# Optimization experiments

Hardware: AMD Instinct MI355X
Metric: run time of the kernel (lower is better)

Reference implementation:

```python
import jax, jax.numpy as jnp
import numpy as np

N_NODES = 50000
N_EDGES = 1_600_000
N_REL = 8
D_IN = 128
D_OUT = 128


def _unique_edges(rng, n_nodes, n_rel, n_edges):
    # Torch module clamps the dense adjacency to 0/1, so duplicate
    # (rel, src, dst) triples collapse; generate unique edges so the
    # edge-list formulation matches exactly.
    m = 2 * n_edges
    src = rng.integers(0, n_nodes, m)
    dst = rng.integers(0, n_nodes, m)
    et = rng.integers(0, n_rel, m)
    key = (et.astype(np.int64) * n_nodes + src) * n_nodes + dst
    _, idx = np.unique(key, return_index=True)
    idx = np.sort(idx)[:n_edges]
    return src[idx], dst[idx], et[idx]


def setup_inputs() -> dict:
    key = jax.random.key(0)
    kx, kw, kr, kb = jax.random.split(key, 4)
    rng = np.random.default_rng(0)
    src, dst, et = _unique_edges(rng, N_NODES, N_REL, N_EDGES)
    bound = 1.0 / np.sqrt(D_OUT)
    return {
        "x": jax.random.normal(kx, (N_NODES, D_IN), dtype=jnp.float32),
        "edge_index": jnp.asarray(np.stack([src, dst]), dtype=jnp.int64),
        "edge_type": jnp.asarray(et, dtype=jnp.int64),
        "weight": jax.random.uniform(kw, (N_REL, D_OUT, D_IN), minval=-bound, maxval=bound, dtype=jnp.float32),
        "root": jax.random.uniform(kr, (D_OUT, D_IN), minval=-bound, maxval=bound, dtype=jnp.float32),
        "bias": jax.random.uniform(kb, (D_OUT,), minval=-bound, maxval=bound, dtype=jnp.float32),
    }


def reference(x, edge_index, edge_type, weight, root, bias):
    # Math identical to: adj[l, src, dst] = 1; adj row-normalized (mean);
    # out = sum_r norm_adj_r @ x @ W_r^T + x @ root^T + bias.
    n_rel, d_out, d_in = weight.shape
    n_nodes = x.shape[0]
    src = edge_index[0]
    dst = edge_index[1]
    seg = (edge_type * n_nodes + src).astype(jnp.int32)  # segment per (rel, node)
    num_seg = n_rel * n_nodes
    # sum of neighbor features per (relation, node): [R*N, d_in]
    agg = jax.ops.segment_sum(x[dst], seg, num_segments=num_seg)
    deg = jax.ops.segment_sum(jnp.ones((src.shape[0],), dtype=x.dtype), seg, num_segments=num_seg)
    norm = jnp.where(deg > 0, 1.0 / deg, 0.0)[:, None]  # mean aggr, nan_to_num(0)
    agg = (agg * norm).reshape(n_rel, n_nodes, d_in)
    out = jnp.einsum('rnd,rod->no', agg, weight)
    out = out + x @ root.T + bias[None]
    return out
```

## Files before the change

kernel.cpp:

```cpp
#include <hip/hip_runtime.h>


#define D 128
#define SCAN_CHUNK 2048
#define SEG_BITS 9
#define SEGS_PER_BUCKET 512
#define NBLK 128
#define NDEG 32

typedef __attribute__((ext_vector_type(8))) short short8;
typedef __attribute__((ext_vector_type(4))) float v4f;
typedef __attribute__((ext_vector_type(2))) float f32x2;
typedef __attribute__((ext_vector_type(4))) unsigned uint4v;

#define GLOAD_LDS16(gptr, lptr) \
    __builtin_amdgcn_global_load_lds((const __attribute__((address_space(1))) void*)(gptr), \
                                     (__attribute__((address_space(3))) void*)(lptr), 16, 0, 0)

__device__ __forceinline__ unsigned short f2b(float f) {
    union { float f; unsigned u; } v; v.f = f;
    unsigned r = v.u + 0x7fffu + ((v.u >> 16) & 1u);
    return (unsigned short)(r >> 16);
}
__device__ __forceinline__ float blo(unsigned u) {
    union { unsigned u; float f; } v; v.u = u << 16; return v.f;
}
__device__ __forceinline__ float bhi(unsigned u) {
    union { unsigned u; float f; } v; v.u = u & 0xffff0000u; return v.f;
}

__global__ void cvt_bf16_all(const float* __restrict__ x, long long nx,
                             const float* __restrict__ w, long long nw,
                             const float* __restrict__ root, long long nr,
                             unsigned short* __restrict__ Abuf,
                             unsigned short* __restrict__ wB, size_t SLs) {
    long long i = ((long long)blockIdx.x * blockDim.x + threadIdx.x) * 4;
    if (i < nx) {
        float4 v = *(const float4*)(x + i);
        uint2 p;
        p.x = (unsigned)f2b(v.x) | ((unsigned)f2b(v.y) << 16);
        p.y = (unsigned)f2b(v.z) | ((unsigned)f2b(v.w) << 16);
        long long n = i >> 7;
        int d = (int)(i & 127);
        size_t o = (size_t)((d >> 5) * 9 + 8) * SLs + (size_t)n * 32 + (d & 31);
        *(uint2*)(Abuf + o) = p;
        return;
    }
    const float* src;
    unsigned short* dst;
    long long j;
    if (i < nx + nw) { src = w; dst = wB; j = i - nx; }
    else if (i < nx + nw + nr) { src = root; dst = wB + nw; j = i - nx - nw; }
    else return;
    float4 v = *(const float4*)(src + j);
    uint2 p;
    p.x = (unsigned)f2b(v.x) | ((unsigned)f2b(v.y) << 16);
    p.y = (unsigned)f2b(v.z) | ((unsigned)f2b(v.w) << 16);
    *(uint2*)(dst + j) = p;
}

__global__ __launch_bounds__(256)
void histA(const int* __restrict__ ei, const int* __restrict__ et,
           int* __restrict__ blockHist, int nE, int nN, int B, int epb) {
    __shared__ int lh[1024];
    const int tid = threadIdx.x;
    for (int b = tid; b < B; b += 256) lh[b] = 0;
    __syncthreads();
    const int base = blockIdx.x * epb;
    const int lim = min(base + epb, nE);
    for (int e = base + tid; e < lim; e += 256) {
        int seg = et[e] * nN + ei[e];
        atomicAdd(&lh[seg >> SEG_BITS], 1);
    }
    __syncthreads();
    for (int b = tid; b < B; b += 256)
        blockHist[b * NBLK + blockIdx.x] = lh[b];
}

__global__ __launch_bounds__(256)
void scan1(const int* __restrict__ in, int* __restrict__ excl,
           int* __restrict__ blockSums, int n) {
    __shared__ int t[256];
    const int tid = threadIdx.x;
    const int base = blockIdx.x * SCAN_CHUNK + tid * 8;
    int v[8];
    int tot = 0;
#pragma unroll
    for (int i = 0; i < 8; i++) {
        v[i] = (base + i < n) ? in[base + i] : 0;
        tot += v[i];
    }
    t[tid] = tot;
    __syncthreads();
    for (int off = 1; off < 256; off <<= 1) {
        int add = (tid >= off) ? t[tid - off] : 0;
        __syncthreads();
        t[tid] += add;
        __syncthreads();
    }
    int run = t[tid] - tot;
#pragma unroll
    for (int i = 0; i < 8; i++) {
        if (base + i < n) excl[base + i] = run;
        run += v[i];
    }
    if (tid == 255) blockSums[blockIdx.x] = t[255];
}

__global__ __launch_bounds__(256)
void scan2(int* __restrict__ blockSums, int nb) {
    __shared__ int t[256];
    const int tid = threadIdx.x;
    int v = (tid < nb) ? blockSums[tid] : 0;
    t[tid] = v;
    __syncthreads();
    for (int off = 1; off < 256; off <<= 1) {
        int add = (tid >= off) ? t[tid - off] : 0;
        __syncthreads();
        t[tid] += add;
        __syncthreads();
    }
    if (tid < nb) blockSums[tid] = t[tid] - v;
}

__global__ __launch_bounds__(256)
void scatterA(const int* __restrict__ ei, const int* __restrict__ et,
              const int* __restrict__ scanned, const int* __restrict__ blockSums,
              unsigned* __restrict__ bucketEdges,
              int nE, int nN, int B, int epb) {
    __shared__ int cur[1024];
    const int tid = threadIdx.x;
    for (int b = tid; b < B; b += 256) {
        int idx = b * NBLK + blockIdx.x;
        cur[b] = scanned[idx] + blockSums[idx >> 11];
    }
    __syncthreads();
    const int base = blockIdx.x * epb;
    const int lim = min(base + epb, nE);
    for (int e = base + tid; e < lim; e += 256) {
        int seg = et[e] * nN + ei[e];
        int bkt = seg >> SEG_BITS;
        unsigned pk = ((unsigned)(seg & (SEGS_PER_BUCKET - 1)) << 16) | (unsigned)ei[nE + e];
        int pos = atomicAdd(&cur[bkt], 1);
        bucketEdges[pos] = pk;
    }
}

__global__ __launch_bounds__(256)
void segOff(const unsigned* __restrict__ bucketEdges, const int* __restrict__ scanned,
            const int* __restrict__ blockSums,
            int4* __restrict__ permRec, unsigned short* __restrict__ sortedDst,
            int* __restrict__ permMax, int nE, int numSeg, int B) {
    __shared__ int lh[SEGS_PER_BUCKET];
    __shared__ int sc[256];
    __shared__ int lcur[SEGS_PER_BUCKET];
    __shared__ int dcnt[256];
    __shared__ int dbase[256];
    __shared__ int smax[32];
    const int tid = threadIdx.x;
    const int b = blockIdx.x;
    const int i0 = b * NBLK;
    const int eBase = scanned[i0] + blockSums[i0 >> 11];
    int eEnd = nE;
    if (b + 1 < B) {
        const int i1 = (b + 1) * NBLK;
        eEnd = scanned[i1] + blockSums[i1 >> 11];
    }
    const int segBase = b * SEGS_PER_BUCKET;
    const int segLim = min(SEGS_PER_BUCKET, numSeg - segBase);

    lh[2 * tid] = 0; lh[2 * tid + 1] = 0;
    dcnt[tid] = 0;
    if (tid < 32) smax[tid] = 0;
    __syncthreads();
    for (int i = eBase + tid; i < eEnd; i += 256)
        atomicAdd(&lh[bucketEdges[i] >> 16], 1);
    __syncthreads();
    const int li0 = 2 * tid, li1 = 2 * tid + 1;
    const int sub = li0 >> 6;
    int a0 = lh[li0], a1 = lh[li1];
    int b0 = min(a0, NDEG - 1), b1 = min(a1, NDEG - 1), r0 = 0, r1 = 0;
    if (li0 < segLim) r0 = atomicAdd(&dcnt[sub * NDEG + b0], 1);
    if (li1 < segLim) r1 = atomicAdd(&dcnt[sub * NDEG + b1], 1);
    sc[tid] = a0 + a1;
    __syncthreads();
    for (int o = 1; o < 256; o <<= 1) {
        int add = (tid >= o) ? sc[tid - o] : 0;
        __syncthreads();
        sc[tid] += add;
        __syncthreads();
    }
    int pairBase = sc[tid] - (a0 + a1);
    int g0 = eBase + pairBase;
    int g1 = g0 + a0;
    lcur[li0] = g0;
    lcur[li1] = g1;
    if (tid < 8) {
        int run = 0;
#pragma unroll
        for (int k = 0; k < NDEG; k++) { dbase[tid * NDEG + k] = run; run += dcnt[tid * NDEG + k]; }
    }
    __syncthreads();
    if (li0 < segLim) {
        int rk = dbase[sub * NDEG + b0] + r0;
        permRec[segBase + sub * 64 + rk] = make_int4(g0, a0, segBase + li0, 0);
        atomicMax(&smax[(sub << 2) + (rk >> 4)], a0);
    }
    if (li1 < segLim) {
        int rk = dbase[sub * NDEG + b1] + r1;
        permRec[segBase + sub * 64 + rk] = make_int4(g1, a1, segBase + li1, 0);
        atomicMax(&smax[(sub << 2) + (rk >> 4)], a1);
    }
    for (int i = eBase + tid; i < eEnd; i += 256) {
        unsigned u = bucketEdges[i];
        int pos = atomicAdd(&lcur[u >> 16], 1);
        sortedDst[pos] = (unsigned short)(u & 0xFFFFu);
    }
    __syncthreads();
    if (tid < 32) permMax[b * 32 + tid] = smax[tid];
}

__global__ __launch_bounds__(256)
void rgcn_gather(const unsigned short* __restrict__ Abase,
                 const unsigned short* __restrict__ sortedDst,
                 const int4* __restrict__ permRec,
                 const int* __restrict__ permMax,
                 unsigned short* __restrict__ Abuf, int nN, int numSeg,
                 size_t SLs, unsigned long long M) {
    const int tid = threadIdx.x;
    const int lane = tid & 63;
    const int idx4 = lane & 3;
    const int grp = lane >> 2;
    const int wv = tid >> 6;
    const int gsi0 = blockIdx.x * 128 + wv * 32 + grp;
    const int gsi1 = gsi0 + 16;
    const int sl = blockIdx.y;
    const bool v0 = (gsi0 < numSeg);
    const bool v1 = (gsi1 < numSeg);

    int4 rc0 = v0 ? permRec[gsi0] : make_int4(0, 0, 0, 0);
    int4 rc1 = v1 ? permRec[gsi1] : make_int4(0, 0, 0, 0);
    int mx0 = v0 ? permMax[gsi0 >> 4] : 0;
    int mx1 = v1 ? permMax[gsi1 >> 4] : 0;
    mx0 = __builtin_amdgcn_readfirstlane(mx0);
    mx1 = __builtin_amdgcn_readfirstlane(mx1);

    const int start0 = rc0.x, cnt0 = v0 ? rc0.y : 0, seg0 = rc0.z;
    const int start1 = rc1.x, cnt1 = v1 ? rc1.y : 0, seg1 = rc1.z;

    f32x2 a0[4], a1[4];
#pragma unroll
    for (int i = 0; i < 4; i++) { a0[i] = (f32x2){0.f, 0.f}; a1[i] = (f32x2){0.f, 0.f}; }

    const unsigned short* xSlab = Abase + (size_t)(sl * 9 + 8) * SLs + idx4 * 8;

    const int mxm = max(mx0, mx1);
    for (int b = 0; b < mxm; b += 4) {
        uint4v w0[4], w1[4];
        int myD0 = 0, myD1 = 0;
        if (b < mx0) myD0 = (b + idx4 < cnt0) ? (int)sortedDst[start0 + b + idx4] : 0;
        if (b < mx1) myD1 = (b + idx4 < cnt1) ? (int)sortedDst[start1 + b + idx4] : 0;
        if (b < mx0) {
#pragma unroll
            for (int j = 0; j < 4; j++) {
                int dst = __shfl(myD0, grp * 4 + j);
                bool act = (b + j < cnt0);
                w0[j] = act ? *(const uint4v*)(xSlab + ((size_t)dst << 5))
                            : (uint4v){0u, 0u, 0u, 0u};
            }
        }
        if (b < mx1) {
#pragma unroll
            for (int j = 0; j < 4; j++) {
                int dst = __shfl(myD1, grp * 4 + j);
                bool act = (b + j < cnt1);
                w1[j] = act ? *(const uint4v*)(xSlab + ((size_t)dst << 5))
                            : (uint4v){0u, 0u, 0u, 0u};
            }
        }
        if (b < mx0) {
#pragma unroll
            for (int j = 0; j < 4; j++) {
                f32x2 t0 = (f32x2){blo(w0[j].x), bhi(w0[j].x)};
                f32x2 t1 = (f32x2){blo(w0[j].y), bhi(w0[j].y)};
                f32x2 t2 = (f32x2){blo(w0[j].z), bhi(w0[j].z)};
                f32x2 t3 = (f32x2){blo(w0[j].w), bhi(w0[j].w)};
                asm("v_pk_add_f32 %0, %0, %1" : "+v"(a0[0]) : "v"(t0));
                asm("v_pk_add_f32 %0, %0, %1" : "+v"(a0[1]) : "v"(t1));
                asm("v_pk_add_f32 %0, %0, %1" : "+v"(a0[2]) : "v"(t2));
                asm("v_pk_add_f32 %0, %0, %1" : "+v"(a0[3]) : "v"(t3));
            }
        }
        if (b < mx1) {
#pragma unroll
            for (int j = 0; j < 4; j++) {
                f32x2 t0 = (f32x2){blo(w1[j].x), bhi(w1[j].x)};
                f32x2 t1 = (f32x2){blo(w1[j].y), bhi(w1[j].y)};
                f32x2 t2 = (f32x2){blo(w1[j].z), bhi(w1[j].z)};
                f32x2 t3 = (f32x2){blo(w1[j].w), bhi(w1[j].w)};
                asm("v_pk_add_f32 %0, %0, %1" : "+v"(a1[0]) : "v"(t0));
                asm("v_pk_add_f32 %0, %0, %1" : "+v"(a1[1]) : "v"(t1));
                asm("v_pk_add_f32 %0, %0, %1" : "+v"(a1[2]) : "v"(t2));
                asm("v_pk_add_f32 %0, %0, %1" : "+v"(a1[3]) : "v"(t3));
            }
        }
    }

    if (v0) {
        float s = cnt0 > 0 ? 1.0f / (float)cnt0 : 0.f;
        const int r = (int)(((unsigned long long)seg0 * M) >> 48);
        const int n = seg0 - r * nN;
        unsigned p0, p1, p2, p3;
        float e0, e1;
        e0 = a0[0].x * s; e1 = a0[0].y * s;
        asm("v_cvt_pk_bf16_f32 %0, %1, %2" : "=v"(p0) : "v"(e0), "v"(e1));
        e0 = a0[1].x * s; e1 = a0[1].y * s;
        asm("v_cvt_pk_bf16_f32 %0, %1, %2" : "=v"(p1) : "v"(e0), "v"(e1));
        e0 = a0[2].x * s; e1 = a0[2].y * s;
        asm("v_cvt_pk_bf16_f32 %0, %1, %2" : "=v"(p2) : "v"(e0), "v"(e1));
        e0 = a0[3].x * s; e1 = a0[3].y * s;
        asm("v_cvt_pk_bf16_f32 %0, %1, %2" : "=v"(p3) : "v"(e0), "v"(e1));
        uint4v pkt = (uint4v){p0, p1, p2, p3};
        __builtin_nontemporal_store(pkt,
            (uint4v*)(Abuf + (size_t)(sl * 9 + r) * SLs + (size_t)n * 32 + idx4 * 8));
    }
    if (v1) {
        float s = cnt1 > 0 ? 1.0f / (float)cnt1 : 0.f;
        const int r = (int)(((unsigned long long)seg1 * M) >> 48);
        const int n = seg1 - r * nN;
        unsigned p0, p1, p2, p3;
        float e0, e1;
        e0 = a1[0].x * s; e1 = a1[0].y * s;
        asm("v_cvt_pk_bf16_f32 %0, %1, %2" : "=v"(p0) : "v"(e0), "v"(e1));
        e0 = a1[1].x * s; e1 = a1[1].y * s;
        asm("v_cvt_pk_bf16_f32 %0, %1, %2" : "=v"(p1) : "v"(e0), "v"(e1));
        e0 = a1[2].x * s; e1 = a1[2].y * s;
        asm("v_cvt_pk_bf16_f32 %0, %1, %2" : "=v"(p2) : "v"(e0), "v"(e1));
        e0 = a1[3].x * s; e1 = a1[3].y * s;
        asm("v_cvt_pk_bf16_f32 %0, %1, %2" : "=v"(p3) : "v"(e0), "v"(e1));
        uint4v pkt = (uint4v){p0, p1, p2, p3};
        __builtin_nontemporal_store(pkt,
            (uint4v*)(Abuf + (size_t)(sl * 9 + r) * SLs + (size_t)n * 32 + idx4 * 8));
    }
}

__global__ __launch_bounds__(256)
void rgcn_gemm_mfma(const unsigned short* __restrict__ A,
                    const unsigned short* __restrict__ wB,
                    const float* __restrict__ bias,
                    float* __restrict__ out, int nN, int nRel, size_t SLs) {
    __shared__ __align__(16) unsigned short As[2][64 * 64];
    __shared__ __align__(16) unsigned short Bs[2][128 * 64];
    const int tid = threadIdx.x;
    const int wave = tid >> 6;
    const int lane = tid & 63;
    const int wm = wave & 1;
    const int wn = wave >> 1;
    const int m16 = lane & 15;
    const int q = lane >> 4;
    const int row0 = blockIdx.x * 64;

    v4f acc[2][4];
#pragma unroll
    for (int i = 0; i < 2; i++)
#pragma unroll
        for (int j = 0; j < 4; j++) acc[i][j] = (v4f){0.f, 0.f, 0.f, 0.f};

    const int sw = m16 & 7;
    int aoff[2][2], boff[4][2];
#pragma unroll
    for (int mt = 0; mt < 2; mt++) {
        int row = wm * 32 + mt * 16 + m16;
#pragma unroll
        for (int kb = 0; kb < 2; kb++)
            aoff[mt][kb] = row * 64 + (((kb * 4 + q) ^ sw) * 8);
    }
#pragma unroll
    for (int nt = 0; nt < 4; nt++) {
        int o = wn * 64 + nt * 16 + m16;
#pragma unroll
        for (int kb = 0; kb < 2; kb++)
            boff[nt][kb] = o * 64 + (((kb * 4 + q) ^ sw) * 8);
    }

    const int l8 = lane >> 3;
    const int gd = (lane & 7) ^ l8;
    const size_t aBaseH0 = (size_t)((gd >> 2) * 9) * SLs
                         + (size_t)(row0 + wave * 16 + l8) * 32 + (gd & 3) * 8;
    const size_t bBase = (size_t)(wave * 32 + l8) * D + gd * 8;

    const int nT = 2 * (nRel + 1);

#define STAGE(buf, t) do { \
        const int s_ = (t) >> 1, h_ = (t) & 1; \
        const unsigned short* ga_ = A + aBaseH0 + (size_t)h_ * 18 * SLs + (size_t)s_ * SLs; \
        const unsigned short* gb_ = wB + (size_t)s_ * (D * D) + h_ * 64 + bBase; \
        GLOAD_LDS16(ga_,        &As[buf][(wave * 2 + 0) * 512]); \
        GLOAD_LDS16(ga_ + 256,  &As[buf][(wave * 2 + 1) * 512]); \
        GLOAD_LDS16(gb_,        &Bs[buf][(wave * 4 + 0) * 512]); \
        GLOAD_LDS16(gb_ + 1024, &Bs[buf][(wave * 4 + 1) * 512]); \
        GLOAD_LDS16(gb_ + 2048, &Bs[buf][(wave * 4 + 2) * 512]); \
        GLOAD_LDS16(gb_ + 3072, &Bs[buf][(wave * 4 + 3) * 512]); \
    } while (0)

    STAGE(0, 0);
    __syncthreads();
    int cur = 0;
    for (int t = 0; t < nT; ++t) {
        if (t + 1 < nT) STAGE(cur ^ 1, t + 1);
        const unsigned short* Ab = As[cur];
        const unsigned short* Bb = Bs[cur];
        short8 a[2][2], b[4][2];
#pragma unroll
        for (int kb = 0; kb < 2; kb++) {
#pragma unroll
            for (int mt = 0; mt < 2; mt++)
                a[mt][kb] = *(const short8*)&Ab[aoff[mt][kb]];
#pragma unroll
            for (int nt = 0; nt < 4; nt++)
                b[nt][kb] = *(const short8*)&Bb[boff[nt][kb]];
        }
#pragma unroll
        for (int kb = 0; kb < 2; kb++)
#pragma unroll
            for (int mt = 0; mt < 2; mt++)
#pragma unroll
                for (int nt = 0; nt < 4; nt++)
                    acc[mt][nt] = __builtin_amdgcn_mfma_f32_16x16x32_bf16(
                        a[mt][kb], b[nt][kb], acc[mt][nt], 0, 0, 0);
        __syncthreads();
        cur ^= 1;
    }
#undef STAGE

#pragma unroll
    for (int mt = 0; mt < 2; mt++) {
#pragma unroll
        for (int nt = 0; nt < 4; nt++) {
            int col = wn * 64 + nt * 16 + m16;
            float bi = bias[col];
#pragma unroll
            for (int reg = 0; reg < 4; reg++) {
                int rrow = row0 + wm * 32 + mt * 16 + q * 4 + reg;
                if (rrow < nN)
                    out[(size_t)rrow * D + col] = acc[mt][nt][reg] + bi;
            }
        }
    }
}

extern "C" void kernel_launch(void* const* d_in, const int* in_sizes, int n_in,
                              void* d_out, int out_size, void* d_ws, size_t ws_size,
                              hipStream_t stream) {
    const float* x    = (const float*)d_in[0];
    const int*   ei   = (const int*)d_in[1];
    const int*   et   = (const int*)d_in[2];
    const float* w    = (const float*)d_in[3];
    const float* root = (const float*)d_in[4];
    const float* bias = (const float*)d_in[5];
    float* out = (float*)d_out;

    const int nN   = in_sizes[0] / D;
    const int nE   = in_sizes[2];
    const int nRel = in_sizes[3] / (D * D);
    const int numSeg = nRel * nN;
    const int B = (numSeg + SEGS_PER_BUCKET - 1) >> SEG_BITS;
    const int nBH = B * NBLK;
    const int epb = (nE + NBLK - 1) / NBLK;
    const int nNalloc = (nN + 63) & ~63;
    const size_t SLs = (size_t)nNalloc * 32;
    const unsigned long long M = ((1ULL << 48) + nN - 1) / nN;

    char* p = (char*)d_ws;
    unsigned* bucketEdges   = (unsigned*)p;        p += (size_t)nE * sizeof(unsigned);
    unsigned short* sortedDst = (unsigned short*)p; p += (size_t)nE * sizeof(unsigned short);
    p = (char*)(((uintptr_t)p + 255) & ~(uintptr_t)255);
    int* blockHist = (int*)p;  p += (size_t)nBH * sizeof(int);
    int* scanned   = (int*)p;  p += (size_t)nBH * sizeof(int);
    int* blockSums = (int*)p;  p += 256 * sizeof(int);
    p = (char*)(((uintptr_t)p + 255) & ~(uintptr_t)255);
    int4* permRec  = (int4*)p; p += (size_t)numSeg * sizeof(int4);
    int* permMax   = (int*)p;  p += (size_t)B * 32 * sizeof(int);
    p = (char*)(((uintptr_t)p + 255) & ~(uintptr_t)255);
    unsigned short* wBc  = (unsigned short*)p;  p += (size_t)(nRel + 1) * D * D * sizeof(unsigned short);
    p = (char*)(((uintptr_t)p + 255) & ~(uintptr_t)255);
    unsigned short* Abuf = (unsigned short*)p;

    const int nScanBlocks = (nBH + SCAN_CHUNK - 1) / SCAN_CHUNK;

    histA<<<NBLK, 256, 0, stream>>>(ei, et, blockHist, nE, nN, B, epb);
    scan1<<<nScanBlocks, 256, 0, stream>>>(blockHist, scanned, blockSums, nBH);
    scan2<<<1, 256, 0, stream>>>(blockSums, nScanBlocks);
    scatterA<<<NBLK, 256, 0, stream>>>(ei, et, scanned, blockSums, bucketEdges, nE, nN, B, epb);
    segOff<<<B, 256, 0, stream>>>(bucketEdges, scanned, blockSums, permRec, sortedDst, permMax,
                                  nE, numSeg, B);

    long long nx = (long long)nN * D;
    long long nw = (long long)nRel * D * D;
    long long nr = (long long)D * D;
    long long ncvt = (nx + nw + nr) / 4;
    cvt_bf16_all<<<(int)((ncvt + 255) / 256), 256, 0, stream>>>(x, nx, w, nw, root, nr,
                                                                Abuf, wBc, SLs);

    dim3 gg((numSeg + 127) / 128, 4);
    rgcn_gather<<<gg, 256, 0, stream>>>(Abuf, sortedDst, permRec, permMax, Abuf, nN, numSeg,
                                        SLs, M);

    rgcn_gemm_mfma<<<(nN + 63) / 64, 256, 0, stream>>>(Abuf, wBc, bias, out, nN, nRel, SLs);
}
```

Before: 272.6 us.

## Enlarge GEMM row tile to 128 and vectorize edge histogram/scatter loads

The MFMA GEMM now computes 128 output rows per block instead of 64. Each wave covers 64 rows with a 4x4 grid of MFMA tiles, so every B-tile fetch is reused across twice as many rows. This costs more accumulator registers and halves the number of blocks. The histogram and bucket-scatter passes now read edge indices as int4, four edges per thread, and the number of partitioning blocks doubles to 256; edges per block are rounded to a multiple of four to keep those loads aligned. Node allocation is padded to 128 to match the new tile.

```diff
diff --git a/kernel.cpp b/kernel.cpp
--- a/kernel.cpp
+++ b/kernel.cpp
@@ -5,7 +5,7 @@
 #define SCAN_CHUNK 2048
 #define SEG_BITS 9
 #define SEGS_PER_BUCKET 512
-#define NBLK 128
+#define NBLK 256
 #define NDEG 32
 
 typedef __attribute__((ext_vector_type(8))) short short8;
@@ -68,9 +68,18 @@
     __syncthreads();
     const int base = blockIdx.x * epb;
     const int lim = min(base + epb, nE);
-    for (int e = base + tid; e < lim; e += 256) {
-        int seg = et[e] * nN + ei[e];
-        atomicAdd(&lh[seg >> SEG_BITS], 1);
+    for (int e = base + tid * 4; e < lim; e += 1024) {
+        if (e + 4 <= lim) {
+            int4 s = *(const int4*)(ei + e);
+            int4 t = *(const int4*)(et + e);
+            atomicAdd(&lh[(t.x * nN + s.x) >> SEG_BITS], 1);
+            atomicAdd(&lh[(t.y * nN + s.y) >> SEG_BITS], 1);
+            atomicAdd(&lh[(t.z * nN + s.z) >> SEG_BITS], 1);
+            atomicAdd(&lh[(t.w * nN + s.w) >> SEG_BITS], 1);
+        } else {
+            for (int k = e; k < lim; k++)
+                atomicAdd(&lh[(et[k] * nN + ei[k]) >> SEG_BITS], 1);
+        }
     }
     __syncthreads();
     for (int b = tid; b < B; b += 256)
@@ -137,12 +146,31 @@
     __syncthreads();
     const int base = blockIdx.x * epb;
     const int lim = min(base + epb, nE);
-    for (int e = base + tid; e < lim; e += 256) {
-        int seg = et[e] * nN + ei[e];
-        int bkt = seg >> SEG_BITS;
-        unsigned pk = ((unsigned)(seg & (SEGS_PER_BUCKET - 1)) << 16) | (unsigned)ei[nE + e];
-        int pos = atomicAdd(&cur[bkt], 1);
-        bucketEdges[pos] = pk;
+    for (int e = base + tid * 4; e < lim; e += 1024) {
+        if (e + 4 <= lim) {
+            int4 s = *(const int4*)(ei + e);
+            int4 t = *(const int4*)(et + e);
+            int4 d = *(const int4*)(ei + nE + e);
+            int sg;
+            sg = t.x * nN + s.x;
+            bucketEdges[atomicAdd(&cur[sg >> SEG_BITS], 1)] =
+                ((unsigned)(sg & (SEGS_PER_BUCKET - 1)) << 16) | (unsigned)d.x;
+            sg = t.y * nN + s.y;
+            bucketEdges[atomicAdd(&cur[sg >> SEG_BITS], 1)] =
+                ((unsigned)(sg & (SEGS_PER_BUCKET - 1)) << 16) | (unsigned)d.y;
+            sg = t.z * nN + s.z;
+            bucketEdges[atomicAdd(&cur[sg >> SEG_BITS], 1)] =
+                ((unsigned)(sg & (SEGS_PER_BUCKET - 1)) << 16) | (unsigned)d.z;
+            sg = t.w * nN + s.w;
+            bucketEdges[atomicAdd(&cur[sg >> SEG_BITS], 1)] =
+                ((unsigned)(sg & (SEGS_PER_BUCKET - 1)) << 16) | (unsigned)d.w;
+        } else {
+            for (int k = e; k < lim; k++) {
+                int sg = et[k] * nN + ei[k];
+                bucketEdges[atomicAdd(&cur[sg >> SEG_BITS], 1)] =
+                    ((unsigned)(sg & (SEGS_PER_BUCKET - 1)) << 16) | (unsigned)ei[nE + k];
+            }
+        }
     }
 }
 
@@ -349,7 +377,7 @@
                     const unsigned short* __restrict__ wB,
                     const float* __restrict__ bias,
                     float* __restrict__ out, int nN, int nRel, size_t SLs) {
-    __shared__ __align__(16) unsigned short As[2][64 * 64];
+    __shared__ __align__(16) unsigned short As[2][128 * 64];
     __shared__ __align__(16) unsigned short Bs[2][128 * 64];
     const int tid = threadIdx.x;
     const int wave = tid >> 6;
@@ -358,19 +386,19 @@
     const int wn = wave >> 1;
     const int m16 = lane & 15;
     const int q = lane >> 4;
-    const int row0 = blockIdx.x * 64;
-
-    v4f acc[2][4];
-#pragma unroll
-    for (int i = 0; i < 2; i++)
+    const int row0 = blockIdx.x * 128;
+
+    v4f acc[4][4];
+#pragma unroll
+    for (int i = 0; i < 4; i++)
 #pragma unroll
         for (int j = 0; j < 4; j++) acc[i][j] = (v4f){0.f, 0.f, 0.f, 0.f};
 
     const int sw = m16 & 7;
-    int aoff[2][2], boff[4][2];
-#pragma unroll
-    for (int mt = 0; mt < 2; mt++) {
-        int row = wm * 32 + mt * 16 + m16;
+    int aoff[4][2], boff[4][2];
+#pragma unroll
+    for (int mt = 0; mt < 4; mt++) {
+        int row = wm * 64 + mt * 16 + m16;
 #pragma unroll
         for (int kb = 0; kb < 2; kb++)
             aoff[mt][kb] = row * 64 + (((kb * 4 + q) ^ sw) * 8);
@@ -385,18 +413,23 @@
 
     const int l8 = lane >> 3;
     const int gd = (lane & 7) ^ l8;
-    const size_t aBaseH0 = (size_t)((gd >> 2) * 9) * SLs
-                         + (size_t)(row0 + wave * 16 + l8) * 32 + (gd & 3) * 8;
+    size_t aB[4];
+#pragma unroll
+    for (int i = 0; i < 4; i++)
+        aB[i] = (size_t)((gd >> 2) * 9) * SLs
+              + (size_t)(row0 + wave * 32 + i * 8 + l8) * 32 + (gd & 3) * 8;
     const size_t bBase = (size_t)(wave * 32 + l8) * D + gd * 8;
 
     const int nT = 2 * (nRel + 1);
 
 #define STAGE(buf, t) do { \
         const int s_ = (t) >> 1, h_ = (t) & 1; \
-        const unsigned short* ga_ = A + aBaseH0 + (size_t)h_ * 18 * SLs + (size_t)s_ * SLs; \
+        const size_t hs_ = (size_t)h_ * 18 * SLs + (size_t)s_ * SLs; \
         const unsigned short* gb_ = wB + (size_t)s_ * (D * D) + h_ * 64 + bBase; \
-        GLOAD_LDS16(ga_,        &As[buf][(wave * 2 + 0) * 512]); \
-        GLOAD_LDS16(ga_ + 256,  &As[buf][(wave * 2 + 1) * 512]); \
+        GLOAD_LDS16(A + aB[0] + hs_, &As[buf][(wave * 4 + 0) * 512]); \
+        GLOAD_LDS16(A + aB[1] + hs_, &As[buf][(wave * 4 + 1) * 512]); \
+        GLOAD_LDS16(A + aB[2] + hs_, &As[buf][(wave * 4 + 2) * 512]); \
+        GLOAD_LDS16(A + aB[3] + hs_, &As[buf][(wave * 4 + 3) * 512]); \
         GLOAD_LDS16(gb_,        &Bs[buf][(wave * 4 + 0) * 512]); \
         GLOAD_LDS16(gb_ + 1024, &Bs[buf][(wave * 4 + 1) * 512]); \
         GLOAD_LDS16(gb_ + 2048, &Bs[buf][(wave * 4 + 2) * 512]); \
@@ -410,38 +443,36 @@
         if (t + 1 < nT) STAGE(cur ^ 1, t + 1);
         const unsigned short* Ab = As[cur];
         const unsigned short* Bb = Bs[cur];
-        short8 a[2][2], b[4][2];
 #pragma unroll
         for (int kb = 0; kb < 2; kb++) {
-#pragma unroll
-            for (int mt = 0; mt < 2; mt++)
-                a[mt][kb] = *(const short8*)&Ab[aoff[mt][kb]];
+            short8 a[4], b[4];
+#pragma unroll
+            for (int mt = 0; mt < 4; mt++)
+                a[mt] = *(const short8*)&Ab[aoff[mt][kb]];
 #pragma unroll
             for (int nt = 0; nt < 4; nt++)
-                b[nt][kb] = *(const short8*)&Bb[boff[nt][kb]];
-        }
-#pragma unroll
-        for (int kb = 0; kb < 2; kb++)
-#pragma unroll
-            for (int mt = 0; mt < 2; mt++)
+                b[nt] = *(const short8*)&Bb[boff[nt][kb]];
+#pragma unroll
+            for (int mt = 0; mt < 4; mt++)
 #pragma unroll
                 for (int nt = 0; nt < 4; nt++)
                     acc[mt][nt] = __builtin_amdgcn_mfma_f32_16x16x32_bf16(
-                        a[mt][kb], b[nt][kb], acc[mt][nt], 0, 0, 0);
+                        a[mt], b[nt], acc[mt][nt], 0, 0, 0);
+        }
         __syncthreads();
         cur ^= 1;
     }
 #undef STAGE
 
 #pragma unroll
-    for (int mt = 0; mt < 2; mt++) {
+    for (int mt = 0; mt < 4; mt++) {
 #pragma unroll
         for (int nt = 0; nt < 4; nt++) {
             int col = wn * 64 + nt * 16 + m16;
             float bi = bias[col];
 #pragma unroll
             for (int reg = 0; reg < 4; reg++) {
-                int rrow = row0 + wm * 32 + mt * 16 + q * 4 + reg;
+                int rrow = row0 + wm * 64 + mt * 16 + q * 4 + reg;
                 if (rrow < nN)
                     out[(size_t)rrow * D + col] = acc[mt][nt][reg] + bi;
             }
@@ -466,8 +497,8 @@
     const int numSeg = nRel * nN;
     const int B = (numSeg + SEGS_PER_BUCKET - 1) >> SEG_BITS;
     const int nBH = B * NBLK;
-    const int epb = (nE + NBLK - 1) / NBLK;
-    const int nNalloc = (nN + 63) & ~63;
+    const int epb = (((nE + NBLK - 1) / NBLK) + 3) & ~3;
+    const int nNalloc = (nN + 127) & ~127;
     const size_t SLs = (size_t)nNalloc * 32;
     const unsigned long long M = ((1ULL << 48) + nN - 1) / nN;
 
@@ -506,5 +537,5 @@
     rgcn_gather<<<gg, 256, 0, stream>>>(Abuf, sortedDst, permRec, permMax, Abuf, nN, numSeg,
                                         SLs, M);
 
-    rgcn_gemm_mfma<<<(nN + 63) / 64, 256, 0, stream>>>(Abuf, wBc, bias, out, nN, nRel, SLs);
-}
+    rgcn_gemm_mfma<<<(nN + 127) / 128, 256, 0, stream>>>(Abuf, wBc, bias, out, nN, nRel, SLs);
+}
```

After: 225.7 us. -17.2%, faster.
